# Optimization experiments

Hardware: AMD Instinct MI355X
Metric: run time of the kernel (lower is better)

Reference implementation:

```python
import jax, jax.numpy as jnp
import numpy as np

N = 10000   # num_nodes
F = 64      # latent_dim
U = 128     # num_units
B = 8       # batch
K = 2       # gcn_step
E = 160000  # edges (avg degree 16)
M = 2 * K + 1  # num_matrices = len(supports)*gcn_step + 1


def setup_inputs() -> dict:
    rng = np.random.default_rng(0)
    rows = rng.integers(0, N, E).astype(np.int32)
    cols = rng.integers(0, N, E).astype(np.int32)
    vals = (rng.random(E).astype(np.float32) + 0.1)
    # random-walk normalization D^{-1} A, per the original utils.calculate_random_walk_matrix
    deg_out = np.zeros(N, np.float32); np.add.at(deg_out, rows, vals)
    deg_in = np.zeros(N, np.float32); np.add.at(deg_in, cols, vals)
    # support1 = (D_out^{-1} A)^T : out[c] += vals/d_out[r] * x[r]  -> dst=cols, src=rows
    w1 = vals / np.maximum(deg_out[rows], 1e-8)
    # support2 = (D_in^{-1} A^T)^T : out[r] += vals/d_in[c] * x[c]  -> dst=rows, src=cols
    w2 = vals / np.maximum(deg_in[cols], 1e-8)

    key = jax.random.key(0)
    ks = jax.random.split(key, 4)

    def xavier(k, shape):
        std = (2.0 / (shape[0] + shape[1])) ** 0.5
        return jax.random.normal(k, shape, jnp.float32) * std

    return {
        'y': jax.random.normal(ks[0], (B, N * F), jnp.float32),
        'W_lat': xavier(ks[1], (M * F, F)),
        'b_lat': jnp.ones((F,), jnp.float32),   # bias_start=1.0, shared (keyed by length)
        'W_units': xavier(ks[2], (M * F, U)),
        'b_units': jnp.zeros((U,), jnp.float32),
        'W_final': xavier(ks[3], (M * U, F)),
        'sup1_w': jnp.asarray(w1),
        'sup2_w': jnp.asarray(w2),
        'edge_rows': jnp.asarray(rows),
        'edge_cols': jnp.asarray(cols),
    }


def _spmm(dst, src, w, x):
    # sparse matmul S @ x with S given as COO edge list; x: (N, Fin, B)
    return jax.ops.segment_sum(w[:, None, None] * x[src], dst, num_segments=N)


def _gconv(x, supports, W, b):
    # x: (B, N, Fin) -> (B, N*Fout); Chebyshev diffusion convolution
    Bsz, n, fin = x.shape
    x0 = jnp.transpose(x, (1, 2, 0))  # (N, Fin, B)
    xs = [x0]
    for dst, src, w in supports:
        xk_2 = x0
        x1 = _spmm(dst, src, w, x0)
        xs.append(x1)
        for _ in range(2, K + 1):
            x2 = 2.0 * _spmm(dst, src, w, x1) - xk_2
            xs.append(x2)
            xk_2, x1 = x1, x2
    X = jnp.stack(xs, axis=-1)                       # (N, Fin, B, M)
    X = jnp.transpose(X, (2, 0, 1, 3)).reshape(Bsz * n, fin * len(xs))  # feature-major, matrix-minor
    out = X @ W + b
    return out.reshape(Bsz, n * W.shape[1])


def reference(y, W_lat, b_lat, W_units, b_units, W_final, sup1_w, sup2_w, edge_rows, edge_cols):
    supports = [(edge_cols, edge_rows, sup1_w), (edge_rows, edge_cols, sup2_w)]
    x = y.reshape(B, N, F)
    # theta gate (bias_start=1.0 via shared b_lat)
    theta = jax.nn.sigmoid(_gconv(x, supports, W_lat, b_lat))
    # ode_func_net: gen_layers=1 hidden gconv + final gconv (final bias is shared b_lat!)
    c = jnp.tanh(_gconv(x, supports, W_units, b_units)).reshape(B, N, U)
    c = jnp.tanh(_gconv(c, supports, W_final, b_lat))
    return -theta * c
```

## Files before the change

### kernel.cpp

```cpp
#include <hip/hip_runtime.h>

#define N_NODES 10000
#define NEDGE 160000
#define NB 80000
#define SCAN_CH 40

typedef unsigned int u32;
typedef unsigned short u16;
typedef __attribute__((ext_vector_type(8))) short short8;
typedef __attribute__((ext_vector_type(4))) float float4v;

__device__ __forceinline__ float bf2f(u16 h) { return __uint_as_float(((u32)h) << 16); }
__device__ __forceinline__ u16 f2bf(float f) {
    u32 u = __float_as_uint(f);
    return (u16)((u + 0x7fffu + ((u >> 16) & 1u)) >> 16);
}
__device__ __forceinline__ float lo16(u32 u) { return __uint_as_float(u << 16); }
__device__ __forceinline__ float hi16(u32 u) { return __uint_as_float(u & 0xffff0000u); }
__device__ __forceinline__ u32 pack2(float a, float b) {
    return (u32)f2bf(a) | (((u32)f2bf(b)) << 16);
}
__device__ __forceinline__ float fast_tanh(float v) {
    return 1.f - 2.f / (__expf(2.f * v) + 1.f);
}

__global__ __launch_bounds__(256) void prep_kernel(
    const float2* __restrict__ y, u32* __restrict__ X0,
    const float* __restrict__ W_lat, const float* __restrict__ W_units,
    u16* __restrict__ bpk12,
    const float* __restrict__ W_final, u16* __restrict__ bpkP,
    int* __restrict__ cnt) {
    int b = blockIdx.x, t = threadIdx.x;
    if (b < 10000) {
        int idx = b * 256 + t;
        int fh = idx & 31;
        int rb = idx >> 5;
        int bb = rb & 7;
        int n = rb >> 3;
        float2 v = y[((size_t)bb * N_NODES + n) * 32 + fh];
        X0[idx] = pack2(v.x, v.y);
    } else if (b < 10240) {
        int idx = (b - 10000) * 256 + t;
        int j = idx & 7;
        int lane = (idx >> 3) & 63;
        int rest = idx >> 9;
        int ct = rest % 12;
        int ks = rest / 12;
        int k = ks * 32 + (lane >> 4) * 8 + j;
        int col = ct * 16 + (lane & 15);
        int wrow = (k % 64) * 5 + (k / 64);
        float v = (col < 64) ? W_lat[wrow * 64 + col] : W_units[wrow * 128 + (col - 64)];
        bpk12[idx] = f2bf(v);
    } else if (b < 10400) {
        int idx = (b - 10240) * 256 + t;
        int j8 = idx & 7;
        int lane = (idx >> 3) & 63;
        int rest = idx >> 9;
        int ct = rest % 20;
        int ks = rest / 20;
        int k = ks * 32 + (lane >> 4) * 8 + j8;
        int col = ct * 16 + (lane & 15);
        int slot = col >> 6, j = col & 63;
        float v;
        if (slot == 0)
            v = W_final[(k * 5 + 0) * 64 + j] - W_final[(k * 5 + 2) * 64 + j] -
                W_final[(k * 5 + 4) * 64 + j];
        else
            v = W_final[(k * 5 + slot) * 64 + j];
        bpkP[idx] = f2bf(v);
    } else {
        int idx = (b - 10400) * 256 + t;
        if (idx < 2 * N_NODES) cnt[idx] = 0;
    }
}

__global__ void count_kernel(const int* __restrict__ rows, const int* __restrict__ cols,
                             int* __restrict__ cnt1, int* __restrict__ cnt2) {
    int e = blockIdx.x * 256 + threadIdx.x;
    if (e < NEDGE) {
        atomicAdd(&cnt1[cols[e]], 1);
        atomicAdd(&cnt2[rows[e]], 1);
    }
}

__global__ void blocksum_kernel(const int* __restrict__ cnt, int* __restrict__ bsums) {
    __shared__ int red[4];
    int arr = blockIdx.x / SCAN_CH;
    int c = blockIdx.x % SCAN_CH;
    int idx = c * 256 + threadIdx.x;
    int v = (idx < N_NODES) ? cnt[arr * N_NODES + idx] : 0;
#pragma unroll
    for (int off = 32; off; off >>= 1) v += __shfl_down(v, off, 64);
    int wv = threadIdx.x >> 6, ln = threadIdx.x & 63;
    if (ln == 0) red[wv] = v;
    __syncthreads();
    if (threadIdx.x == 0) bsums[blockIdx.x] = red[0] + red[1] + red[2] + red[3];
}

__global__ void scanmid_kernel(int* __restrict__ bsums, int* __restrict__ rowptr1,
                               int* __restrict__ rowptr2) {
    __shared__ int lds[128];
    int t = threadIdx.x;
    int seg = t >> 6, pos = t & 63;
    int v = (pos < SCAN_CH) ? bsums[seg * SCAN_CH + pos] : 0;
    lds[t] = v;
    __syncthreads();
    for (int off = 1; off < 64; off <<= 1) {
        int add = (pos >= off) ? lds[t - off] : 0;
        __syncthreads();
        lds[t] += add;
        __syncthreads();
    }
    if (pos < SCAN_CH) bsums[seg * SCAN_CH + pos] = pos ? lds[t - 1] : 0;
    if (t == 0) { rowptr1[N_NODES] = NEDGE; rowptr2[N_NODES] = NEDGE; }
}

__global__ void scanapply_kernel(int* __restrict__ cnt, const int* __restrict__ bsums,
                                 int* __restrict__ rowptr1, int* __restrict__ rowptr2) {
    __shared__ int lds[256];
    int arr = blockIdx.x / SCAN_CH;
    int c = blockIdx.x % SCAN_CH;
    int idx = c * 256 + threadIdx.x;
    bool ok = idx < N_NODES;
    int v = ok ? cnt[arr * N_NODES + idx] : 0;
    int t = threadIdx.x;
    lds[t] = v;
    __syncthreads();
    for (int off = 1; off < 256; off <<= 1) {
        int add = (t >= off) ? lds[t - off] : 0;
        __syncthreads();
        lds[t] += add;
        __syncthreads();
    }
    int excl = lds[t] - v + bsums[blockIdx.x];
    if (ok) {
        int* rp = arr ? rowptr2 : rowptr1;
        rp[idx] = excl;
        cnt[arr * N_NODES + idx] = excl;
    }
}

__global__ void scatter_kernel(const int* __restrict__ rows, const int* __restrict__ cols,
                               const float* __restrict__ w1, const float* __restrict__ w2,
                               int* __restrict__ cur1, int* __restrict__ cur2,
                               int2* __restrict__ edges1, int2* __restrict__ edges2) {
    int e = blockIdx.x * 256 + threadIdx.x;
    if (e < NEDGE) {
        int r = rows[e], c = cols[e];
        int p1 = atomicAdd(&cur1[c], 1);
        edges1[p1] = make_int2(r, __float_as_int(w1[e]));
        int p2 = atomicAdd(&cur2[r], 1);
        edges2[p2] = make_int2(c, __float_as_int(w2[e]));
    }
}

__device__ __forceinline__ void gather_row(const u32* __restrict__ Xin,
                                           const int* __restrict__ rp,
                                           const int2* __restrict__ eg,
                                           int n, int lane, float* acc) {
    int e0 = rp[n], e1 = rp[n + 1];
    for (int base = e0; base < e1; base += 64) {
        int m = min(64, e1 - base);
        int2 me = make_int2(0, 0);
        if (lane < m) me = eg[base + lane];
        for (int j = 0; j < m; j++) {
            int src = __shfl(me.x, j, 64);
            float w = __int_as_float(__shfl(me.y, j, 64));
            uint4 u = *(const uint4*)(Xin + (size_t)src * 256 + lane * 4);
            acc[0] += w * lo16(u.x); acc[1] += w * hi16(u.x);
            acc[2] += w * lo16(u.y); acc[3] += w * hi16(u.y);
            acc[4] += w * lo16(u.z); acc[5] += w * hi16(u.z);
            acc[6] += w * lo16(u.w); acc[7] += w * hi16(u.w);
        }
    }
}

__global__ __launch_bounds__(256) void spmm2_kernel(
    const u32* __restrict__ XinA, const u32* __restrict__ XprevA, u32* __restrict__ XoutA,
    const u32* __restrict__ XinB, const u32* __restrict__ XprevB, u32* __restrict__ XoutB,
    const int* __restrict__ rowptr1, const int2* __restrict__ edges1,
    const int* __restrict__ rowptr2, const int2* __restrict__ edges2,
    float alpha, float beta) {
    int lane = threadIdx.x & 63;
    int v = blockIdx.x * 4 + (threadIdx.x >> 6);
    if (v >= 2 * N_NODES) return;
    bool hB = v >= N_NODES;
    int n = hB ? v - N_NODES : v;
    const u32* Xin = hB ? XinB : XinA;
    const u32* Xprev = hB ? XprevB : XprevA;
    u32* Xout = hB ? XoutB : XoutA;
    const int* rp = hB ? rowptr2 : rowptr1;
    const int2* eg = hB ? edges2 : edges1;

    float acc[8] = {0.f, 0.f, 0.f, 0.f, 0.f, 0.f, 0.f, 0.f};
    gather_row(Xin, rp, eg, n, lane, acc);

    size_t o = (size_t)n * 256 + lane * 4;
    if (beta != 0.f) {
        uint4 p = *(const uint4*)(Xprev + o);
        acc[0] = alpha * acc[0] + beta * lo16(p.x); acc[1] = alpha * acc[1] + beta * hi16(p.x);
        acc[2] = alpha * acc[2] + beta * lo16(p.y); acc[3] = alpha * acc[3] + beta * hi16(p.y);
        acc[4] = alpha * acc[4] + beta * lo16(p.z); acc[5] = alpha * acc[5] + beta * hi16(p.z);
        acc[6] = alpha * acc[6] + beta * lo16(p.w); acc[7] = alpha * acc[7] + beta * hi16(p.w);
    } else {
#pragma unroll
        for (int i = 0; i < 8; i++) acc[i] *= alpha;
    }
    uint4 r;
    r.x = pack2(acc[0], acc[1]);
    r.y = pack2(acc[2], acc[3]);
    r.z = pack2(acc[4], acc[5]);
    r.w = pack2(acc[6], acc[7]);
    *(uint4*)(Xout + o) = r;
}

__global__ __launch_bounds__(256) void spmm_final_kernel(
    const u32* __restrict__ T1, const u32* __restrict__ T2,
    const u32* __restrict__ Q, const u32* __restrict__ theta,
    const int* __restrict__ rowptr1, const int2* __restrict__ edges1,
    const int* __restrict__ rowptr2, const int2* __restrict__ edges2,
    float* __restrict__ outF) {
    int lane = threadIdx.x & 63;
    int n = blockIdx.x * 4 + (threadIdx.x >> 6);
    if (n >= N_NODES) return;

    float acc[8] = {0.f, 0.f, 0.f, 0.f, 0.f, 0.f, 0.f, 0.f};
    gather_row(T1, rowptr1, edges1, n, lane, acc);
    gather_row(T2, rowptr2, edges2, n, lane, acc);

    size_t o = (size_t)n * 256 + lane * 4;
    uint4 q = *(const uint4*)(Q + o);
    uint4 th = *(const uint4*)(theta + o);
    float res[8];
    res[0] = -lo16(th.x) * fast_tanh(lo16(q.x) + acc[0]);
    res[1] = -hi16(th.x) * fast_tanh(hi16(q.x) + acc[1]);
    res[2] = -lo16(th.y) * fast_tanh(lo16(q.y) + acc[2]);
    res[3] = -hi16(th.y) * fast_tanh(hi16(q.y) + acc[3]);
    res[4] = -lo16(th.z) * fast_tanh(lo16(q.z) + acc[4]);
    res[5] = -hi16(th.z) * fast_tanh(hi16(q.z) + acc[5]);
    res[6] = -lo16(th.w) * fast_tanh(lo16(q.w) + acc[6]);
    res[7] = -hi16(th.w) * fast_tanh(hi16(q.w) + acc[7]);
    int b = lane >> 3;
    int f0 = ((lane * 4) & 31) * 2;
    float* dst = outF + (size_t)b * (N_NODES * 64) + (size_t)n * 64 + f0;
    *(float4*)(dst) = make_float4(res[0], res[1], res[2], res[3]);
    *(float4*)(dst + 4) = make_float4(res[4], res[5], res[6], res[7]);
}

struct Slabs { const u16* p[5]; };

template <int FIN, int NM, int NOUT, int MODE>
__global__ __launch_bounds__(256) void gemm_kernel(
    Slabs A, const u16* __restrict__ Bp, const float* __restrict__ bias1,
    const float* __restrict__ bias2, u16* __restrict__ O1, u16* __restrict__ O2) {
    constexpr int K = NM * FIN;
    constexpr int KS = K / 32;
    constexpr int CT = NOUT / 16;
    int lane = threadIdx.x & 63;
    int wave = threadIdx.x >> 6;
    int rowBase = blockIdx.x * 128 + wave * 32;
    int mrow = lane & 15;
    int kq = lane >> 4;

    short8 a0[KS], a1[KS];
#pragma unroll
    for (int ks = 0; ks < KS; ks++) {
        int k = ks * 32 + kq * 8;
        int m = k / FIN;
        int koff = k % FIN;
        const u16* abase = A.p[m] + (size_t)(rowBase + mrow) * FIN + koff;
        a0[ks] = *(const short8*)(abase);
        a1[ks] = *(const short8*)(abase + 16 * FIN);
    }

    float4v acc[2][CT];
#pragma unroll
    for (int s = 0; s < 2; s++)
#pragma unroll
        for (int c = 0; c < CT; c++) acc[s][c] = (float4v){0.f, 0.f, 0.f, 0.f};

#pragma unroll
    for (int ks = 0; ks < KS; ks++) {
        const u16* bbase = Bp + ((size_t)(ks * CT) * 64 + lane) * 8;
#pragma unroll
        for (int ct = 0; ct < CT; ct++) {
            short8 b = *(const short8*)(bbase + (size_t)ct * 64 * 8);
            acc[0][ct] = __builtin_amdgcn_mfma_f32_16x16x32_bf16(a0[ks], b, acc[0][ct], 0, 0, 0);
            acc[1][ct] = __builtin_amdgcn_mfma_f32_16x16x32_bf16(a1[ks], b, acc[1][ct], 0, 0, 0);
        }
    }

#pragma unroll
    for (int sub = 0; sub < 2; sub++) {
        int rowq = rowBase + sub * 16 + kq * 4;
#pragma unroll
        for (int ct = 0; ct < CT; ct++) {
            int col = ct * 16 + mrow;
            float bsv;
            if (MODE == 0) bsv = (col < 64) ? bias1[col] : 0.f;
            else bsv = (col < 64) ? bias1[col] : bias2[col - 64];
#pragma unroll
            for (int i = 0; i < 4; i++) {
                float v = acc[sub][ct][i] + bsv;
                int r = rowq + i;
                if (MODE == 0) {
                    O1[(size_t)(col >> 6) * ((size_t)NB * 64) + (size_t)r * 64 + (col & 63)] = f2bf(v);
                } else {
                    if (col < 64) {
                        v = 1.f / (1.f + __expf(-v));
                        O1[(size_t)r * 64 + col] = f2bf(v);
                    } else {
                        O2[(size_t)r * 128 + (col - 64)] = f2bf(fast_tanh(v));
                    }
                }
            }
        }
    }
}

extern "C" void kernel_launch(void* const* d_in, const int* in_sizes, int n_in,
                              void* d_out, int out_size, void* d_ws, size_t ws_size,
                              hipStream_t stream) {
    const float* y     = (const float*)d_in[0];
    const float* W_lat = (const float*)d_in[1];
    const float* b_lat = (const float*)d_in[2];
    const float* W_units = (const float*)d_in[3];
    const float* b_units = (const float*)d_in[4];
    const float* W_final = (const float*)d_in[5];
    const float* sup1w = (const float*)d_in[6];
    const float* sup2w = (const float*)d_in[7];
    const int* rows    = (const int*)d_in[8];
    const int* cols    = (const int*)d_in[9];
    float* out = (float*)d_out;

    char* ws = (char*)d_ws;
    size_t off = 0;
    auto alloc = [&](size_t bytes) -> void* {
        void* p = ws + off;
        off += (bytes + 511) & ~(size_t)511;
        return p;
    };
    int* rowptr1 = (int*)alloc((N_NODES + 1) * 4);
    int* rowptr2 = (int*)alloc((N_NODES + 1) * 4);
    int* cnt = (int*)alloc((size_t)2 * N_NODES * 4);
    int* cnt1 = cnt;
    int* cnt2 = cnt + N_NODES;
    int* bsums = (int*)alloc(2 * SCAN_CH * 4);
    int2* edges1 = (int2*)alloc((size_t)NEDGE * 8);
    int2* edges2 = (int2*)alloc((size_t)NEDGE * 8);
    u16* bpk12 = (u16*)alloc((size_t)61440 * 2);
    u16* bpkP = (u16*)alloc((size_t)40960 * 2);
    u16* theta = (u16*)alloc((size_t)NB * 64 * 2);
    u16* S = (u16*)alloc((size_t)5 * NB * 64 * 2);
    u16* H0 = (u16*)alloc((size_t)NB * 128 * 2);
    u16* T1 = (u16*)alloc((size_t)NB * 64 * 2);
    u16* T2 = (u16*)alloc((size_t)NB * 64 * 2);
    u16* P = S;

    const size_t SLAB = (size_t)NB * 64;

    prep_kernel<<<10479, 256, 0, stream>>>((const float2*)y, (u32*)S, W_lat, W_units,
                                           bpk12, W_final, bpkP, cnt);
    count_kernel<<<(NEDGE + 255) / 256, 256, 0, stream>>>(rows, cols, cnt1, cnt2);
    blocksum_kernel<<<2 * SCAN_CH, 256, 0, stream>>>(cnt, bsums);
    scanmid_kernel<<<1, 128, 0, stream>>>(bsums, rowptr1, rowptr2);
    scanapply_kernel<<<2 * SCAN_CH, 256, 0, stream>>>(cnt, bsums, rowptr1, rowptr2);
    scatter_kernel<<<(NEDGE + 255) / 256, 256, 0, stream>>>(rows, cols, sup1w, sup2w,
                                                            cnt1, cnt2, edges1, edges2);

    const u32* S0 = (const u32*)S;
    u32* X1 = (u32*)(S + 1 * SLAB);
    u32* X2 = (u32*)(S + 2 * SLAB);
    u32* X3 = (u32*)(S + 3 * SLAB);
    u32* X4 = (u32*)(S + 4 * SLAB);
    spmm2_kernel<<<5000, 256, 0, stream>>>(S0, nullptr, X1, S0, nullptr, X3,
                                           rowptr1, edges1, rowptr2, edges2, 1.f, 0.f);
    spmm2_kernel<<<5000, 256, 0, stream>>>(X1, S0, X2, X3, S0, X4,
                                           rowptr1, edges1, rowptr2, edges2, 2.f, -1.f);

    Slabs SX;
    for (int m = 0; m < 5; m++) SX.p[m] = S + (size_t)m * SLAB;
    gemm_kernel<64, 5, 192, 1><<<625, 256, 0, stream>>>(SX, bpk12, b_lat, b_units, theta, H0);

    Slabs SH;
    SH.p[0] = H0;
    gemm_kernel<128, 1, 320, 0><<<625, 256, 0, stream>>>(SH, bpkP, b_lat, nullptr, P, nullptr);

    const u32* Q  = (const u32*)(P + 0 * SLAB);
    const u32* P1 = (const u32*)(P + 1 * SLAB);
    const u32* P2 = (const u32*)(P + 2 * SLAB);
    const u32* P3 = (const u32*)(P + 3 * SLAB);
    const u32* P4 = (const u32*)(P + 4 * SLAB);
    spmm2_kernel<<<5000, 256, 0, stream>>>(P2, (const u32*)P1, (u32*)T1,
                                           P4, (const u32*)P3, (u32*)T2,
                                           rowptr1, edges1, rowptr2, edges2, 2.f, 1.f);
    spmm_final_kernel<<<2500, 256, 0, stream>>>((const u32*)T1, (const u32*)T2, Q,
                                                (const u32*)theta,
                                                rowptr1, edges1, rowptr2, edges2, out);
}
```

Baseline: 377.5 us.

## Unroll SpMM gather by four and shrink GEMM tiles with column splitting

The SpMM gather loop now issues four independent row loads per iteration before accumulating, which raises memory-level parallelism on the irregular neighbor reads. The GEMM kernels move from 32 rows per wave to 16 rows per wave. The second GEMM also splits its output columns across two blocks, so the launch has more, smaller blocks for better occupancy and fewer registers. In exchange, the B-matrix loads and A reads are repeated across the split blocks, and each MFMA B fragment is reused only once instead of twice.

```diff
diff --git a/kernel.cpp b/kernel.cpp
--- a/kernel.cpp
+++ b/kernel.cpp
@@ -154,6 +154,13 @@
     }
 }
 
+__device__ __forceinline__ void gacc(float* acc, float w, uint4 u) {
+    acc[0] += w * lo16(u.x); acc[1] += w * hi16(u.x);
+    acc[2] += w * lo16(u.y); acc[3] += w * hi16(u.y);
+    acc[4] += w * lo16(u.z); acc[5] += w * hi16(u.z);
+    acc[6] += w * lo16(u.w); acc[7] += w * hi16(u.w);
+}
+
 __device__ __forceinline__ void gather_row(const u32* __restrict__ Xin,
                                            const int* __restrict__ rp,
                                            const int2* __restrict__ eg,
@@ -163,14 +170,30 @@
         int m = min(64, e1 - base);
         int2 me = make_int2(0, 0);
         if (lane < m) me = eg[base + lane];
-        for (int j = 0; j < m; j++) {
+        int j = 0;
+        for (; j + 4 <= m; j += 4) {
+            int s0 = __shfl(me.x, j, 64);
+            int s1 = __shfl(me.x, j + 1, 64);
+            int s2 = __shfl(me.x, j + 2, 64);
+            int s3 = __shfl(me.x, j + 3, 64);
+            float w0 = __int_as_float(__shfl(me.y, j, 64));
+            float w1 = __int_as_float(__shfl(me.y, j + 1, 64));
+            float w2 = __int_as_float(__shfl(me.y, j + 2, 64));
+            float w3 = __int_as_float(__shfl(me.y, j + 3, 64));
+            uint4 u0 = *(const uint4*)(Xin + (size_t)s0 * 256 + lane * 4);
+            uint4 u1 = *(const uint4*)(Xin + (size_t)s1 * 256 + lane * 4);
+            uint4 u2 = *(const uint4*)(Xin + (size_t)s2 * 256 + lane * 4);
+            uint4 u3 = *(const uint4*)(Xin + (size_t)s3 * 256 + lane * 4);
+            gacc(acc, w0, u0);
+            gacc(acc, w1, u1);
+            gacc(acc, w2, u2);
+            gacc(acc, w3, u3);
+        }
+        for (; j < m; j++) {
             int src = __shfl(me.x, j, 64);
             float w = __int_as_float(__shfl(me.y, j, 64));
             uint4 u = *(const uint4*)(Xin + (size_t)src * 256 + lane * 4);
-            acc[0] += w * lo16(u.x); acc[1] += w * hi16(u.x);
-            acc[2] += w * lo16(u.y); acc[3] += w * hi16(u.y);
-            acc[4] += w * lo16(u.z); acc[5] += w * hi16(u.z);
-            acc[6] += w * lo16(u.w); acc[7] += w * hi16(u.w);
+            gacc(acc, w, u);
         }
     }
 }
@@ -249,69 +272,59 @@
 
 struct Slabs { const u16* p[5]; };
 
-template <int FIN, int NM, int NOUT, int MODE>
+template <int FIN, int NM, int NOUT, int NSPLIT, int MODE>
 __global__ __launch_bounds__(256) void gemm_kernel(
     Slabs A, const u16* __restrict__ Bp, const float* __restrict__ bias1,
     const float* __restrict__ bias2, u16* __restrict__ O1, u16* __restrict__ O2) {
     constexpr int K = NM * FIN;
     constexpr int KS = K / 32;
-    constexpr int CT = NOUT / 16;
+    constexpr int CTT = NOUT / 16;
+    constexpr int CT = CTT / NSPLIT;
     int lane = threadIdx.x & 63;
     int wave = threadIdx.x >> 6;
-    int rowBase = blockIdx.x * 128 + wave * 32;
+    int rowBase = (blockIdx.x / NSPLIT) * 64 + wave * 16;
+    int ctBase = (blockIdx.x % NSPLIT) * CT;
     int mrow = lane & 15;
     int kq = lane >> 4;
 
-    short8 a0[KS], a1[KS];
+    float4v acc[CT];
+#pragma unroll
+    for (int c = 0; c < CT; c++) acc[c] = (float4v){0.f, 0.f, 0.f, 0.f};
+
 #pragma unroll
     for (int ks = 0; ks < KS; ks++) {
         int k = ks * 32 + kq * 8;
         int m = k / FIN;
         int koff = k % FIN;
-        const u16* abase = A.p[m] + (size_t)(rowBase + mrow) * FIN + koff;
-        a0[ks] = *(const short8*)(abase);
-        a1[ks] = *(const short8*)(abase + 16 * FIN);
-    }
-
-    float4v acc[2][CT];
-#pragma unroll
-    for (int s = 0; s < 2; s++)
-#pragma unroll
-        for (int c = 0; c < CT; c++) acc[s][c] = (float4v){0.f, 0.f, 0.f, 0.f};
-
-#pragma unroll
-    for (int ks = 0; ks < KS; ks++) {
-        const u16* bbase = Bp + ((size_t)(ks * CT) * 64 + lane) * 8;
-#pragma unroll
-        for (int ct = 0; ct < CT; ct++) {
-            short8 b = *(const short8*)(bbase + (size_t)ct * 64 * 8);
-            acc[0][ct] = __builtin_amdgcn_mfma_f32_16x16x32_bf16(a0[ks], b, acc[0][ct], 0, 0, 0);
-            acc[1][ct] = __builtin_amdgcn_mfma_f32_16x16x32_bf16(a1[ks], b, acc[1][ct], 0, 0, 0);
-        }
-    }
-
-#pragma unroll
-    for (int sub = 0; sub < 2; sub++) {
-        int rowq = rowBase + sub * 16 + kq * 4;
-#pragma unroll
-        for (int ct = 0; ct < CT; ct++) {
-            int col = ct * 16 + mrow;
-            float bsv;
-            if (MODE == 0) bsv = (col < 64) ? bias1[col] : 0.f;
-            else bsv = (col < 64) ? bias1[col] : bias2[col - 64];
-#pragma unroll
-            for (int i = 0; i < 4; i++) {
-                float v = acc[sub][ct][i] + bsv;
-                int r = rowq + i;
-                if (MODE == 0) {
-                    O1[(size_t)(col >> 6) * ((size_t)NB * 64) + (size_t)r * 64 + (col & 63)] = f2bf(v);
+        short8 a = *(const short8*)(A.p[m] + (size_t)(rowBase + mrow) * FIN + koff);
+        short8 b[CT];
+#pragma unroll
+        for (int ct = 0; ct < CT; ct++)
+            b[ct] = *(const short8*)(Bp + ((size_t)(ks * CTT + ctBase + ct) * 64 + lane) * 8);
+#pragma unroll
+        for (int ct = 0; ct < CT; ct++)
+            acc[ct] = __builtin_amdgcn_mfma_f32_16x16x32_bf16(a, b[ct], acc[ct], 0, 0, 0);
+    }
+
+    int rowq = rowBase + kq * 4;
+#pragma unroll
+    for (int ct = 0; ct < CT; ct++) {
+        int col = (ctBase + ct) * 16 + mrow;
+        float bsv;
+        if (MODE == 0) bsv = (col < 64) ? bias1[col] : 0.f;
+        else bsv = (col < 64) ? bias1[col] : bias2[col - 64];
+#pragma unroll
+        for (int i = 0; i < 4; i++) {
+            float v = acc[ct][i] + bsv;
+            int r = rowq + i;
+            if (MODE == 0) {
+                O1[(size_t)(col >> 6) * ((size_t)NB * 64) + (size_t)r * 64 + (col & 63)] = f2bf(v);
+            } else {
+                if (col < 64) {
+                    v = 1.f / (1.f + __expf(-v));
+                    O1[(size_t)r * 64 + col] = f2bf(v);
                 } else {
-                    if (col < 64) {
-                        v = 1.f / (1.f + __expf(-v));
-                        O1[(size_t)r * 64 + col] = f2bf(v);
-                    } else {
-                        O2[(size_t)r * 128 + (col - 64)] = f2bf(fast_tanh(v));
-                    }
+                    O2[(size_t)r * 128 + (col - 64)] = f2bf(fast_tanh(v));
                 }
             }
         }
@@ -380,11 +393,11 @@
 
     Slabs SX;
     for (int m = 0; m < 5; m++) SX.p[m] = S + (size_t)m * SLAB;
-    gemm_kernel<64, 5, 192, 1><<<625, 256, 0, stream>>>(SX, bpk12, b_lat, b_units, theta, H0);
+    gemm_kernel<64, 5, 192, 1, 1><<<1250, 256, 0, stream>>>(SX, bpk12, b_lat, b_units, theta, H0);
 
     Slabs SH;
     SH.p[0] = H0;
-    gemm_kernel<128, 1, 320, 0><<<625, 256, 0, stream>>>(SH, bpkP, b_lat, nullptr, P, nullptr);
+    gemm_kernel<128, 1, 320, 2, 0><<<2500, 256, 0, stream>>>(SH, bpkP, b_lat, nullptr, P, nullptr);
 
     const u32* Q  = (const u32*)(P + 0 * SLAB);
     const u32* P1 = (const u32*)(P + 1 * SLAB);
```

Result: faster. 348.0 us (-7.8%).
